# Optimization experiments

Measured on AMD Instinct MI355X. Metric: run time of the kernel, lower is better.

## Reference

```python
import jax, jax.numpy as jnp
import numpy as np

B, S, IN_DIM, OUT_DIM, NUM_BASIS = 2, 512, 64, 64, 8
LN_EPS = 1e-05
TWO_PI = 2.0 * np.pi


def setup_inputs() -> dict:
    key = jax.random.key(0)
    k_x, k_k, k_m, k_r, k_p = jax.random.split(key, 5)
    x = jax.random.normal(k_x, (B, S, IN_DIM), dtype=jnp.float32)
    k = jax.random.randint(k_k, (B, S), 0, S, dtype=jnp.int64)
    # nn.Linear weights are (out, in); inits per reset_parameters()
    M = jax.random.uniform(k_m, (OUT_DIM, IN_DIM), jnp.float32, -0.5, 0.5)
    # in_dim == out_dim -> R = I + 0.01 * randn
    R = jnp.eye(OUT_DIM, IN_DIM, dtype=jnp.float32) + 0.01 * jax.random.normal(k_r, (OUT_DIM, IN_DIM), dtype=jnp.float32)
    P = jax.random.uniform(k_p, (OUT_DIM, OUT_DIM, NUM_BASIS), jnp.float32, -0.1, 0.1)
    gamma = jnp.ones((IN_DIM,), dtype=jnp.float32)
    beta = jnp.zeros((IN_DIM,), dtype=jnp.float32)
    # periods[i,j,g] = i*(out*nb) + j*nb + g + 2  == arange + 2
    periods = (jnp.arange(OUT_DIM * OUT_DIM * NUM_BASIS, dtype=jnp.float32) + 2.0).reshape(OUT_DIM, OUT_DIM, NUM_BASIS)
    return {"x": x, "k": k, "M": M, "R": R, "P": P, "gamma": gamma, "beta": beta, "periods": periods}


def reference(x, k, M, R, P, gamma, beta, periods):
    # LayerNorm over last dim (biased variance, eps inside sqrt)
    mu = jnp.mean(x, axis=-1, keepdims=True)
    var = jnp.mean(jnp.square(x - mu), axis=-1, keepdims=True)
    ln_x = (x - mu) * jax.lax.rsqrt(var + LN_EPS) * gamma + beta
    x_proj = jnp.einsum('bsj,oj->bso', ln_x, M)   # (B,S,out)
    res = jnp.einsum('bsj,oj->bso', ln_x, R)      # (B,S,out)
    # cos(2*pi*k / periods[i,j,g]) broadcast to (B,S,out,out,nb)
    kf = k.astype(x.dtype)[:, :, None, None, None]
    cos_terms = jnp.cos(TWO_PI * kf / periods)
    # Nk[b,s,i] = sum_{j,g} P[i,j,g] * x_proj[b,s,j] * cos_terms[b,s,i,j,g]
    Nk = jnp.einsum('bsijg,ijg,bsj->bsi', cos_terms, P, x_proj)
    return res + Nk
```

## Files before the change

kernel.cpp:

```cpp
#include <hip/hip_runtime.h>


constexpr int BATCH = 2;
constexpr int SEQ   = 512;
constexpr int DIM   = 64;
constexpr int NB    = 8;
constexpr int ROWS  = BATCH * SEQ;
constexpr float LN_EPS = 1e-5f;

__global__ __launch_bounds__(256) void desc_fused(
    const float* __restrict__ x,
    const int*   __restrict__ kk,
    const float* __restrict__ M,
    const float* __restrict__ R,
    const float* __restrict__ P,
    const float* __restrict__ gamma,
    const float* __restrict__ beta,
    const float* __restrict__ periods,
    float* __restrict__ out)
{
    const int r0 = blockIdx.x * 2;
    const int t  = threadIdx.x;

    __shared__ float ln_s [2][DIM];
    __shared__ float xp_s [2][DIM];
    __shared__ float res_s[2][DIM];

    if (t < 2 * DIM) {
        const int rr   = t >> 6;
        const int lane = t & 63;
        float xv = x[(r0 + rr) * DIM + lane];
        float s1 = xv, s2 = xv * xv;
        #pragma unroll
        for (int off = 32; off > 0; off >>= 1) {
            s1 += __shfl_xor(s1, off, 64);
            s2 += __shfl_xor(s2, off, 64);
        }
        float mu  = s1 * (1.0f / DIM);
        float var = s2 * (1.0f / DIM) - mu * mu;
        ln_s[rr][lane] = (xv - mu) * rsqrtf(var + LN_EPS) * gamma[lane] + beta[lane];
    }
    __syncthreads();

    {
        const int g  = t >> 6;
        const int rr = g & 1;
        const int o  = t & 63;
        const float4* W4 = reinterpret_cast<const float4*>(((g < 2) ? M : R) + o * DIM);
        const float4* L4 = reinterpret_cast<const float4*>(ln_s[rr]);
        float acc = 0.f;
        #pragma unroll
        for (int j4 = 0; j4 < DIM / 4; ++j4) {
            float4 w = W4[j4];
            float4 l = L4[j4];
            acc += w.x * l.x + w.y * l.y + w.z * l.z + w.w * l.w;
        }
        if (g < 2) xp_s[rr][o] = acc; else res_s[rr][o] = acc;
    }
    __syncthreads();

    const int   i    = t >> 2;
    const int   part = t & 3;
    const float kf0  = (float)kk[r0];
    const float kf1  = (float)kk[r0 + 1];

    float acc0 = 0.f, acc1 = 0.f;

    #pragma unroll 4
    for (int jj = 0; jj < 16; ++jj) {
        const int j    = jj * 4 + part;
        const int base = (i * DIM + j) * NB;
        float4 p0 = *reinterpret_cast<const float4*>(P + base);
        float4 p1 = *reinterpret_cast<const float4*>(P + base + 4);
        float4 q0 = *reinterpret_cast<const float4*>(periods + base);
        float4 q1 = *reinterpret_cast<const float4*>(periods + base + 4);

        float s0 = 0.f, s1 = 0.f;
        #pragma unroll
        for (int e = 0; e < 8; ++e) {
            float pe = (e < 4) ? ((const float*)&p0)[e] : ((const float*)&p1)[e - 4];
            float qe = (e < 4) ? ((const float*)&q0)[e] : ((const float*)&q1)[e - 4];
            float rp = __builtin_amdgcn_rcpf(qe);
            float c0 = __builtin_amdgcn_cosf(__builtin_amdgcn_fractf(kf0 * rp));
            float c1 = __builtin_amdgcn_cosf(__builtin_amdgcn_fractf(kf1 * rp));
            s0 = fmaf(pe, c0, s0);
            s1 = fmaf(pe, c1, s1);
        }
        acc0 = fmaf(xp_s[0][j], s0, acc0);
        acc1 = fmaf(xp_s[1][j], s1, acc1);
    }

    acc0 += __shfl_xor(acc0, 1, 64);
    acc0 += __shfl_xor(acc0, 2, 64);
    acc1 += __shfl_xor(acc1, 1, 64);
    acc1 += __shfl_xor(acc1, 2, 64);

    if (part == 0) {
        out[(r0    ) * DIM + i] = res_s[0][i] + acc0;
        out[(r0 + 1) * DIM + i] = res_s[1][i] + acc1;
    }
}

extern "C" void kernel_launch(void* const* d_in, const int* in_sizes, int n_in,
                              void* d_out, int out_size, void* d_ws, size_t ws_size,
                              hipStream_t stream)
{
    const float* x       = (const float*)d_in[0];
    const int*   kk      = (const int*)  d_in[1];
    const float* M       = (const float*)d_in[2];
    const float* R       = (const float*)d_in[3];
    const float* P       = (const float*)d_in[4];
    const float* gamma   = (const float*)d_in[5];
    const float* beta    = (const float*)d_in[6];
    const float* periods = (const float*)d_in[7];
    float* out = (float*)d_out;

    desc_fused<<<ROWS / 2, 256, 0, stream>>>(x, kk, M, R, P, gamma, beta, periods, out);
}
```

Before: 79.63 us.

## Process four rows per block and split output dim across block pairs

Each block now handles four sequence rows and half of the output indices, with the grid laid out as row-groups times two halves. The rcp of each period and the P/periods loads are shared across four rows instead of two, which cuts global traffic and reciprocal work per cosine. In exchange, LayerNorm and the full M projection are computed redundantly by both halves, and the per-thread loop now evaluates four cosines per term, which raises register pressure.

New measurement: 80.65 us. About the same (+1.3%).

```diff
diff --git a/kernel.cpp b/kernel.cpp
--- a/kernel.cpp
+++ b/kernel.cpp
@@ -6,6 +6,8 @@
 constexpr int DIM   = 64;
 constexpr int NB    = 8;
 constexpr int ROWS  = BATCH * SEQ;
+constexpr int RPB   = 4;
+constexpr int IHALF = 32;
 constexpr float LN_EPS = 1e-5f;
 
 __global__ __launch_bounds__(256) void desc_fused(
@@ -19,14 +21,16 @@
     const float* __restrict__ periods,
     float* __restrict__ out)
 {
-    const int r0 = blockIdx.x * 2;
+    const int rg = blockIdx.x >> 1;
+    const int ih = blockIdx.x & 1;
+    const int r0 = rg * RPB;
     const int t  = threadIdx.x;
 
-    __shared__ float ln_s [2][DIM];
-    __shared__ float xp_s [2][DIM];
-    __shared__ float res_s[2][DIM];
+    __shared__ float ln_s [RPB][DIM];
+    __shared__ float xp_s [RPB][DIM];
+    __shared__ float res_s[RPB][IHALF];
 
-    if (t < 2 * DIM) {
+    {
         const int rr   = t >> 6;
         const int lane = t & 63;
         float xv = x[(r0 + rr) * DIM + lane];
@@ -43,10 +47,9 @@
     __syncthreads();
 
     {
-        const int g  = t >> 6;
-        const int rr = g & 1;
+        const int rr = t >> 6;
         const int o  = t & 63;
-        const float4* W4 = reinterpret_cast<const float4*>(((g < 2) ? M : R) + o * DIM);
+        const float4* W4 = reinterpret_cast<const float4*>(M + o * DIM);
         const float4* L4 = reinterpret_cast<const float4*>(ln_s[rr]);
         float acc = 0.f;
         #pragma unroll
@@ -55,49 +58,82 @@
             float4 l = L4[j4];
             acc += w.x * l.x + w.y * l.y + w.z * l.z + w.w * l.w;
         }
-        if (g < 2) xp_s[rr][o] = acc; else res_s[rr][o] = acc;
+        xp_s[rr][o] = acc;
+    }
+    if (t < RPB * IHALF) {
+        const int rr = t >> 5;
+        const int ol = t & 31;
+        const float4* W4 = reinterpret_cast<const float4*>(R + (ih * IHALF + ol) * DIM);
+        const float4* L4 = reinterpret_cast<const float4*>(ln_s[rr]);
+        float acc = 0.f;
+        #pragma unroll
+        for (int j4 = 0; j4 < DIM / 4; ++j4) {
+            float4 w = W4[j4];
+            float4 l = L4[j4];
+            acc += w.x * l.x + w.y * l.y + w.z * l.z + w.w * l.w;
+        }
+        res_s[rr][ol] = acc;
     }
     __syncthreads();
 
-    const int   i    = t >> 2;
-    const int   part = t & 3;
-    const float kf0  = (float)kk[r0];
-    const float kf1  = (float)kk[r0 + 1];
+    const int i_local = t >> 3;
+    const int part    = t & 7;
+    const int i_glob  = ih * IHALF + i_local;
 
-    float acc0 = 0.f, acc1 = 0.f;
+    const float kf0 = (float)kk[r0];
+    const float kf1 = (float)kk[r0 + 1];
+    const float kf2 = (float)kk[r0 + 2];
+    const float kf3 = (float)kk[r0 + 3];
 
-    #pragma unroll 4
-    for (int jj = 0; jj < 16; ++jj) {
-        const int j    = jj * 4 + part;
-        const int base = (i * DIM + j) * NB;
-        float4 p0 = *reinterpret_cast<const float4*>(P + base);
-        float4 p1 = *reinterpret_cast<const float4*>(P + base + 4);
-        float4 q0 = *reinterpret_cast<const float4*>(periods + base);
-        float4 q1 = *reinterpret_cast<const float4*>(periods + base + 4);
+    float acc0 = 0.f, acc1 = 0.f, acc2 = 0.f, acc3 = 0.f;
 
-        float s0 = 0.f, s1 = 0.f;
-        #pragma unroll
-        for (int e = 0; e < 8; ++e) {
-            float pe = (e < 4) ? ((const float*)&p0)[e] : ((const float*)&p1)[e - 4];
-            float qe = (e < 4) ? ((const float*)&q0)[e] : ((const float*)&q1)[e - 4];
-            float rp = __builtin_amdgcn_rcpf(qe);
-            float c0 = __builtin_amdgcn_cosf(__builtin_amdgcn_fractf(kf0 * rp));
-            float c1 = __builtin_amdgcn_cosf(__builtin_amdgcn_fractf(kf1 * rp));
-            s0 = fmaf(pe, c0, s0);
-            s1 = fmaf(pe, c1, s1);
+    #pragma unroll 2
+    for (int jj = 0; jj < 8; ++jj) {
+        const int j    = jj * 8 + part;
+        const int base = (i_glob * DIM + j) * NB;
+        const float4 p0 = *reinterpret_cast<const float4*>(P + base);
+        const float4 p1 = *reinterpret_cast<const float4*>(P + base + 4);
+        const float4 q0 = *reinterpret_cast<const float4*>(periods + base);
+        const float4 q1 = *reinterpret_cast<const float4*>(periods + base + 4);
+
+        float s0 = 0.f, s1 = 0.f, s2 = 0.f, s3 = 0.f;
+
+        #define DESC_TERM(PE, QE)                                               \
+        {                                                                       \
+            const float rp_ = __builtin_amdgcn_rcpf(QE);                        \
+            s0 = fmaf(PE, __builtin_amdgcn_cosf(__builtin_amdgcn_fractf(kf0 * rp_)), s0); \
+            s1 = fmaf(PE, __builtin_amdgcn_cosf(__builtin_amdgcn_fractf(kf1 * rp_)), s1); \
+            s2 = fmaf(PE, __builtin_amdgcn_cosf(__builtin_amdgcn_fractf(kf2 * rp_)), s2); \
+            s3 = fmaf(PE, __builtin_amdgcn_cosf(__builtin_amdgcn_fractf(kf3 * rp_)), s3); \
         }
+        DESC_TERM(p0.x, q0.x)
+        DESC_TERM(p0.y, q0.y)
+        DESC_TERM(p0.z, q0.z)
+        DESC_TERM(p0.w, q0.w)
+        DESC_TERM(p1.x, q1.x)
+        DESC_TERM(p1.y, q1.y)
+        DESC_TERM(p1.z, q1.z)
+        DESC_TERM(p1.w, q1.w)
+        #undef DESC_TERM
+
         acc0 = fmaf(xp_s[0][j], s0, acc0);
         acc1 = fmaf(xp_s[1][j], s1, acc1);
+        acc2 = fmaf(xp_s[2][j], s2, acc2);
+        acc3 = fmaf(xp_s[3][j], s3, acc3);
     }
 
-    acc0 += __shfl_xor(acc0, 1, 64);
-    acc0 += __shfl_xor(acc0, 2, 64);
-    acc1 += __shfl_xor(acc1, 1, 64);
-    acc1 += __shfl_xor(acc1, 2, 64);
+    #pragma unroll
+    for (int off = 1; off < 8; off <<= 1) {
+        acc0 += __shfl_xor(acc0, off, 64);
+        acc1 += __shfl_xor(acc1, off, 64);
+        acc2 += __shfl_xor(acc2, off, 64);
+        acc3 += __shfl_xor(acc3, off, 64);
+    }
 
-    if (part == 0) {
-        out[(r0    ) * DIM + i] = res_s[0][i] + acc0;
-        out[(r0 + 1) * DIM + i] = res_s[1][i] + acc1;
+    if (part < RPB) {
+        const float accp = (part == 0) ? acc0 : (part == 1) ? acc1
+                         : (part == 2) ? acc2 : acc3;
+        out[(r0 + part) * DIM + i_glob] = res_s[part][i_local] + accp;
     }
 }
 
@@ -115,5 +151,5 @@
     const float* periods = (const float*)d_in[7];
     float* out = (float*)d_out;
 
-    desc_fused<<<ROWS / 2, 256, 0, stream>>>(x, kk, M, R, P, gamma, beta, periods, out);
+    desc_fused<<<(ROWS / RPB) * 2, 256, 0, stream>>>(x, kk, M, R, P, gamma, beta, periods, out);
 }
```
